# Kernel optimization log

Measured on AMD Instinct MI355X. Metric: run time of the kernel, lower is better.

Reference implementation:

```python
import jax, jax.numpy as jnp
import numpy as np

NUM_HEADS = 16
HEAD_DIM = 64
HIDDEN = NUM_HEADS * HEAD_DIM  # 1024
B, S = 2, 2048
INV_NORM = 1.0 / np.sqrt(HEAD_DIM)


def setup_inputs() -> dict:
    key = jax.random.key(0)
    ks = jax.random.split(key, 8)
    hidden_states = jax.random.normal(ks[0], (1, B, S, HIDDEN), dtype=jnp.float32)
    residual = jax.random.normal(ks[1], (B, S, HIDDEN), dtype=jnp.float32)
    # ALiBi bias per (batch*head) broadcast over query positions: [B*H, 1, S]
    slopes = 2.0 ** (-8.0 * (jnp.arange(1, NUM_HEADS + 1, dtype=jnp.float32) / NUM_HEADS))
    pos = jnp.arange(S, dtype=jnp.float32)
    alibi = (slopes[:, None] * pos[None, :])[None]  # [1, H, S]
    alibi = jnp.broadcast_to(alibi, (B, NUM_HEADS, S)).reshape(B * NUM_HEADS, 1, S)
    # causal mask: True = masked out
    attention_mask = jnp.triu(jnp.ones((S, S), dtype=jnp.bool_), k=1)[None, None]  # [1,1,S,S]
    attention_mask = jnp.broadcast_to(attention_mask, (B, 1, S, S))
    W_qkv = jax.random.normal(ks[2], (3 * HIDDEN, HIDDEN), dtype=jnp.float32) * 0.02
    b_qkv = jax.random.normal(ks[3], (3 * HIDDEN,), dtype=jnp.float32) * 0.02
    W_dense = jax.random.normal(ks[4], (HIDDEN, HIDDEN), dtype=jnp.float32) * 0.02
    b_dense = jax.random.normal(ks[5], (HIDDEN,), dtype=jnp.float32) * 0.02
    return {
        "hidden_states": hidden_states,
        "residual": residual,
        "alibi": alibi,
        "attention_mask": attention_mask,
        "W_qkv": W_qkv,
        "b_qkv": b_qkv,
        "W_dense": W_dense,
        "b_dense": b_dense,
    }


def reference(hidden_states, residual, alibi, attention_mask, W_qkv, b_qkv, W_dense, b_dense):
    x = hidden_states[0]  # [B, S, H]
    b, s, _ = x.shape
    fused = x @ W_qkv.T + b_qkv  # [B, S, 3H]
    # Bloom interleaved split: [B, S, nh, 3, hd]
    qkv = fused.reshape(b, s, NUM_HEADS, 3, HEAD_DIM)
    q = jnp.transpose(qkv[..., 0, :], (0, 2, 1, 3))  # [B, nh, S, hd]
    k = jnp.transpose(qkv[..., 1, :], (0, 2, 1, 3))
    v = jnp.transpose(qkv[..., 2, :], (0, 2, 1, 3))
    # baddbmm: alibi + inv_norm * q @ k^T
    scores = jnp.einsum("bhqd,bhkd->bhqk", q, k) * INV_NORM
    scores = scores + alibi.reshape(b, NUM_HEADS, 1, s)  # [B, nh, S, S]
    neg_min = jnp.finfo(scores.dtype).min
    scores = jnp.where(attention_mask, neg_min, scores)
    probs = jax.nn.softmax(scores.astype(jnp.float32), axis=-1).astype(x.dtype)
    ctx = jnp.einsum("bhqk,bhkd->bhqd", probs, v)  # [B, nh, S, hd]
    ctx = jnp.transpose(ctx, (0, 2, 1, 3)).reshape(b, s, HIDDEN)  # merge_heads
    out = ctx @ W_dense.T + b_dense
    return out + residual  # dropout_add, eval mode
```

## Files before the change

kernel.cpp:

```cpp
#include <hip/hip_runtime.h>
#include <hip/hip_bf16.h>

#define NUM_HEADS 16
#define HEAD_DIM  64
#define HIDDEN    1024
#define BATCH     2
#define SEQ       2048
#define K_DIM     1024
#define INV_NORM  0.125f
#define LOG2E     1.4426950408889634f
#define IN2       (INV_NORM * LOG2E)

typedef __attribute__((ext_vector_type(4)))  float f32x4;
typedef __attribute__((ext_vector_type(16))) float f32x16;
typedef __attribute__((ext_vector_type(8)))  short bf16x8;
typedef __attribute__((ext_vector_type(4)))  unsigned int u32x4;
typedef __attribute__((ext_vector_type(2)))  unsigned int u32x2;
typedef unsigned short u16;

__device__ inline u16 f2bf(float f) {
    __hip_bfloat16 h = __float2bfloat16(f);
    return __builtin_bit_cast(u16, h);
}
__device__ inline float bf2f(u16 u) {
    unsigned int v = ((unsigned int)u) << 16;
    return __builtin_bit_cast(float, v);
}

__device__ inline f32x16 mfma32(bf16x8 a, bf16x8 b, f32x16 c) {
    return __builtin_amdgcn_mfma_f32_32x32x16_bf16(a, b, c, 0, 0, 0);
}

__device__ inline void gl_lds16(const u16* g, u16* s) {
    __builtin_amdgcn_global_load_lds(
        (const __attribute__((address_space(1))) unsigned int*)g,
        (__attribute__((address_space(3))) unsigned int*)s, 16, 0, 0);
}

__device__ inline void pack8(const float* src, u16* dst) {
    const float4 v0 = *reinterpret_cast<const float4*>(src);
    const float4 v1 = *reinterpret_cast<const float4*>(src + 4);
    ushort4 o0, o1;
    o0.x = f2bf(v0.x); o0.y = f2bf(v0.y); o0.z = f2bf(v0.z); o0.w = f2bf(v0.w);
    o1.x = f2bf(v1.x); o1.y = f2bf(v1.y); o1.z = f2bf(v1.z); o1.w = f2bf(v1.w);
    *reinterpret_cast<ushort4*>(dst)     = o0;
    *reinterpret_cast<ushort4*>(dst + 4) = o1;
}
__global__ __launch_bounds__(256) void cvt_all(
        const float* __restrict__ x, const float* __restrict__ wq,
        const float* __restrict__ wd,
        u16* __restrict__ xb, u16* __restrict__ wqb, u16* __restrict__ wdb) {
    int t = blockIdx.x * 256 + threadIdx.x;
    if (t < 524288) {
        int mt = t >> 12, rem = t & 4095;
        int kblk = rem >> 6, hf = (rem >> 5) & 1, ra = rem & 31;
        pack8(x + ((size_t)(mt * 32 + ra)) * K_DIM + kblk * 16 + hf * 8,
              xb + (size_t)t * 8);
    } else if (t < 917504) {
        int t2 = t - 524288;
        int nt = t2 >> 12, rem = t2 & 4095;
        int kblk = rem >> 6, hf = (rem >> 5) & 1, ra = rem & 31;
        pack8(wq + ((size_t)(nt * 32 + ra)) * K_DIM + kblk * 16 + hf * 8,
              wqb + (size_t)t2 * 8);
    } else {
        int i = (t - 917504) * 8;
        pack8(wd + i, wdb + i);
    }
}

#define QLOAD(P, kb) {                                                        \
    P##x0 = *reinterpret_cast<const bf16x8*>(pa0 + (size_t)(kb) * 512);       \
    P##x1 = *reinterpret_cast<const bf16x8*>(pa1 + (size_t)(kb) * 512);       \
    P##y0 = *reinterpret_cast<const bf16x8*>(pb0 + (size_t)(kb) * 512);       \
    P##y1 = *reinterpret_cast<const bf16x8*>(pb1 + (size_t)(kb) * 512);       \
    P##x2 = *reinterpret_cast<const bf16x8*>(pa0 + (size_t)(kb + 1) * 512);   \
    P##x3 = *reinterpret_cast<const bf16x8*>(pa1 + (size_t)(kb + 1) * 512);   \
    P##y2 = *reinterpret_cast<const bf16x8*>(pb0 + (size_t)(kb + 1) * 512);   \
    P##y3 = *reinterpret_cast<const bf16x8*>(pb1 + (size_t)(kb + 1) * 512);   \
}
#define QSTEP(P) {                                                            \
    acc[0][0] = mfma32(P##x0, P##y0, acc[0][0]);                              \
    acc[0][1] = mfma32(P##x0, P##y1, acc[0][1]);                              \
    acc[1][0] = mfma32(P##x1, P##y0, acc[1][0]);                              \
    acc[1][1] = mfma32(P##x1, P##y1, acc[1][1]);                              \
    acc[0][0] = mfma32(P##x2, P##y2, acc[0][0]);                              \
    acc[0][1] = mfma32(P##x2, P##y3, acc[0][1]);                              \
    acc[1][0] = mfma32(P##x3, P##y2, acc[1][0]);                              \
    acc[1][1] = mfma32(P##x3, P##y3, acc[1][1]);                              \
}
__global__ __launch_bounds__(256) void gemm_qkv(
        const u16* __restrict__ Af, const u16* __restrict__ Bf,
        const float* __restrict__ bias,
        u16* __restrict__ qo, u16* __restrict__ ko2, u16* __restrict__ vTo) {
    int lin = blockIdx.x;
    int g = lin & 7, i2 = lin >> 3;
    const int mblk = ((g & 3) * 8 + (i2 & 7)) * 128;
    const int nblk = ((g >> 2) * 12 + (i2 >> 3)) * 128;
    const int tid = threadIdx.x;
    const int w = tid >> 6, lane = tid & 63;
    const int la = lane & 31, hi = lane >> 5;
    const int wr = w >> 1, wc = w & 1;
    const int mt0 = (mblk >> 5) + wr * 2;
    const int nt0 = (nblk >> 5) + wc * 2;
    const u16* pa0 = Af + (size_t)mt0 * 64 * 512 + lane * 8;
    const u16* pa1 = pa0 + 64 * 512;
    const u16* pb0 = Bf + (size_t)nt0 * 64 * 512 + lane * 8;
    const u16* pb1 = pb0 + 64 * 512;
    f32x16 acc[2][2] = {};
    bf16x8 ax0, ax1, ax2, ax3, ay0, ay1, ay2, ay3;
    bf16x8 bx0, bx1, bx2, bx3, by0, by1, by2, by3;
    QLOAD(a, 0)
    #pragma unroll 4
    for (int kb = 0; kb < 64; kb += 4) {
        const int n1 = (kb + 2 < 62) ? kb + 2 : 62;
        QLOAD(b, n1)
        QSTEP(a)
        const int n2 = (kb + 4 < 62) ? kb + 4 : 62;
        QLOAD(a, n2)
        QSTEP(b)
    }
    #pragma unroll
    for (int mi = 0; mi < 2; ++mi)
    #pragma unroll
    for (int ni = 0; ni < 2; ++ni) {
        int c = nblk + wc * 64 + ni * 32 + la;
        int h = c / 192, rem = c - h * 192;
        int which = rem >> 6, d = rem & 63;
        float bv = bias[c];
        #pragma unroll
        for (int r = 0; r < 16; ++r) {
            int m = mblk + wr * 64 + mi * 32 + (r & 3) + 8 * (r >> 2) + 4 * hi;
            int bb = m >> 11, s = m & (SEQ - 1);
            int bh = bb * NUM_HEADS + h;
            int t = s >> 5;
            size_t tb = ((size_t)(bh * 64 + t)) * 2048;
            u16 o = f2bf(acc[mi][ni][r] + bv);
            if (which == 2) {
                int dblk = d >> 5, ra = d & 31;
                int k = s & 31, ks = k >> 4, hf = (k >> 3) & 1, e = k & 7;
                vTo[tb + (dblk * 2 + ks) * 512 + hf * 256 + ra * 8 + e] = o;
            } else {
                int kk = d >> 4, hf = (d >> 3) & 1, e = d & 7, ra = s & 31;
                size_t off = tb + kk * 512 + hf * 256 + ra * 8 + e;
                if (which == 0) qo[off] = o;
                else            ko2[off] = o;
            }
        }
    }
}

__global__ __launch_bounds__(256) void gemm_dense(
        const u16* __restrict__ A, const u16* __restrict__ W,
        const float* __restrict__ bias, const float* __restrict__ residual,
        float* __restrict__ out) {
    __shared__ u16 As[64 * 64];
    __shared__ u16 Bs[128 * 64];
    int lin = blockIdx.x;
    int g = lin & 7, i2 = lin >> 3;
    const int mblk = (g * 8 + (i2 & 7)) * 64;
    const int nblk = (i2 >> 3) * 128;
    const int tid = threadIdx.x;
    const int w = tid >> 6, l = tid & 63;
    const int la = l & 31, hi = l >> 5;
    const int wr = w & 1, wc = w >> 1;
    const int kperm = (((l & 7) ^ (l >> 3)) << 3);
    const u16* gA = A + (size_t)(mblk + w * 16 + (l >> 3)) * K_DIM + kperm;
    const u16* gB = W + (size_t)(nblk + w * 32 + (l >> 3)) * K_DIM + kperm;
    const int sca = (la & 7) << 3;
    f32x16 acc2[2] = {};
    for (int kt = 0; kt < 16; ++kt) {
        const int ko = kt * 64;
        gl_lds16(gA + ko,              &As[(w * 16) * 64]);
        gl_lds16(gA + ko + 8 * K_DIM,  &As[(w * 16 + 8) * 64]);
        #pragma unroll
        for (int i = 0; i < 4; ++i)
            gl_lds16(gB + i * 8 * K_DIM + ko, &Bs[(w * 32 + i * 8) * 64]);
        asm volatile("s_waitcnt vmcnt(0)" ::: "memory");
        __syncthreads();
        const u16* pA = &As[(wr * 32 + la) * 64];
        const u16* pB = &Bs[(wc * 64 + la) * 64];
        #pragma unroll
        for (int kk = 0; kk < 4; ++kk) {
            const int co = (kk * 16 + hi * 8) ^ sca;
            bf16x8 a0 = *reinterpret_cast<const bf16x8*>(pA + co);
            bf16x8 b0 = *reinterpret_cast<const bf16x8*>(pB + co);
            bf16x8 b1 = *reinterpret_cast<const bf16x8*>(pB + 32 * 64 + co);
            acc2[0] = mfma32(a0, b0, acc2[0]);
            acc2[1] = mfma32(a0, b1, acc2[1]);
        }
        __syncthreads();
    }
    #pragma unroll
    for (int ni = 0; ni < 2; ++ni) {
        int c = nblk + wc * 64 + ni * 32 + la;
        float bv = bias[c];
        #pragma unroll
        for (int r = 0; r < 16; ++r) {
            int m = mblk + wr * 32 + (r & 3) + 8 * (r >> 2) + 4 * hi;
            out[(size_t)m * HIDDEN + c] = acc2[ni][r] + bv + residual[(size_t)m * HIDDEN + c];
        }
    }
}

__global__ __launch_bounds__(256) void norms(
        const u16* __restrict__ Kf, const u16* __restrict__ Qf,
        float* __restrict__ knp, float* __restrict__ qn,
        unsigned int* __restrict__ ctr) {
    if (blockIdx.x == 0 && threadIdx.x < 8) ctr[threadIdx.x] = 0;
    __shared__ float red[256];
    const int bh = blockIdx.x >> 3;
    const int s  = (blockIdx.x & 7) * 256 + threadIdx.x;
    const size_t tb = ((size_t)(bh * 64 + (s >> 5))) * 2048 + (s & 31) * 8;
    float ssk = 0.f, ssq = 0.f;
    #pragma unroll
    for (int kk = 0; kk < 4; ++kk)
    #pragma unroll
    for (int hf = 0; hf < 2; ++hf) {
        bf16x8 v = *reinterpret_cast<const bf16x8*>(Kf + tb + kk * 512 + hf * 256);
        bf16x8 u = *reinterpret_cast<const bf16x8*>(Qf + tb + kk * 512 + hf * 256);
        #pragma unroll
        for (int e = 0; e < 8; ++e) {
            float fk = bf2f((u16)v[e]);
            float fq = bf2f((u16)u[e]);
            ssk = fmaf(fk, fk, ssk);
            ssq = fmaf(fq, fq, ssq);
        }
    }
    float mq = ssq;
    #pragma unroll
    for (int off = 1; off <= 16; off <<= 1) mq = fmaxf(mq, __shfl_xor(mq, off));
    if ((threadIdx.x & 31) == 0)
        qn[(size_t)bh * 64 + (s >> 5)] = sqrtf(mq);
    red[threadIdx.x] = ssk;
    __syncthreads();
    for (int off = 128; off; off >>= 1) {
        if (threadIdx.x < (unsigned)off)
            red[threadIdx.x] = fmaxf(red[threadIdx.x], red[threadIdx.x + off]);
        __syncthreads();
    }
    if (threadIdx.x == 0) knp[blockIdx.x] = sqrtf(red[0]);
}

#define LOADT(P, tt) {                                                        \
    const u16* kp_ = kbase + (size_t)(tt) * 2048;                             \
    P##k0 = *reinterpret_cast<const bf16x8*>(kp_);                            \
    P##k1 = *reinterpret_cast<const bf16x8*>(kp_ + 512);                      \
    P##k2 = *reinterpret_cast<const bf16x8*>(kp_ + 1024);                     \
    P##k3 = *reinterpret_cast<const bf16x8*>(kp_ + 1536);                     \
    const u16* vp_ = vbase + (size_t)(tt) * 2048;                             \
    P##v0 = *reinterpret_cast<const bf16x8*>(vp_);                            \
    P##v1 = *reinterpret_cast<const bf16x8*>(vp_ + 512);                      \
    P##v2 = *reinterpret_cast<const bf16x8*>(vp_ + 1024);                     \
    P##v3 = *reinterpret_cast<const bf16x8*>(vp_ + 1536);                     \
}

#define STEP(P, N, tcur, tnxt, DIAG) {                                        \
    f32x16 sca_ = {}, scb_ = {};                                              \
    sca_ = mfma32(P##k0, qf0, sca_);                                          \
    scb_ = mfma32(P##k1, qf1, scb_);                                          \
    sca_ = mfma32(P##k2, qf2, sca_);                                          \
    scb_ = mfma32(P##k3, qf3, scb_);                                          \
    LOADT(N, tnxt)                                                            \
    const float Dt_ = slope2 * (float)((tcur) * 32 - qw);                     \
    float p[16];                                                              \
    _Pragma("unroll")                                                         \
    for (int r = 0; r < 16; ++r)                                              \
        p[r] = __builtin_amdgcn_exp2f(fmaf(sca_[r] + scb_[r], IN2, cl[r] + Dt_)); \
    if (DIAG) {                                                               \
        _Pragma("unroll")                                                     \
        for (int r = 0; r < 16; ++r) {                                        \
            int kr_ = (r & 3) + 8 * (r >> 2) + 4 * hi;                        \
            if (kr_ > la) p[r] = 0.f;                                         \
        }                                                                     \
    }                                                                         \
    l_i += ((p[0] + p[1]) + (p[2] + p[3])) + ((p[4] + p[5]) + (p[6] + p[7]))  \
         + ((p[8] + p[9]) + (p[10] + p[11])) + ((p[12] + p[13]) + (p[14] + p[15])); \
    unsigned pk_[8];                                                          \
    _Pragma("unroll")                                                         \
    for (int m = 0; m < 4; ++m) {                                             \
        unsigned b0_ = __builtin_bit_cast(unsigned, p[4 * m])     + 0x8000u;  \
        unsigned b1_ = __builtin_bit_cast(unsigned, p[4 * m + 1]) + 0x8000u;  \
        unsigned b2_ = __builtin_bit_cast(unsigned, p[4 * m + 2]) + 0x8000u;  \
        unsigned b3_ = __builtin_bit_cast(unsigned, p[4 * m + 3]) + 0x8000u;  \
        pk_[2 * m]     = __builtin_amdgcn_perm(b1_, b0_, 0x07060302u);        \
        pk_[2 * m + 1] = __builtin_amdgcn_perm(b3_, b2_, 0x07060302u);        \
    }                                                                         \
    u32x2 r0_ = __builtin_amdgcn_permlane32_swap(pk_[0], pk_[2], false, false); \
    u32x2 r1_ = __builtin_amdgcn_permlane32_swap(pk_[1], pk_[3], false, false); \
    u32x2 r2_ = __builtin_amdgcn_permlane32_swap(pk_[4], pk_[6], false, false); \
    u32x2 r3_ = __builtin_amdgcn_permlane32_swap(pk_[5], pk_[7], false, false); \
    u32x4 pb0_, pb1_;                                                         \
    pb0_[0] = r0_[0]; pb0_[1] = r1_[0]; pb0_[2] = r0_[1]; pb0_[3] = r1_[1];   \
    pb1_[0] = r2_[0]; pb1_[1] = r3_[0]; pb1_[2] = r2_[1]; pb1_[3] = r3_[1];   \
    bf16x8 pf0_ = __builtin_bit_cast(bf16x8, pb0_);                           \
    bf16x8 pf1_ = __builtin_bit_cast(bf16x8, pb1_);                           \
    o0 = mfma32(P##v0, pf0_, o0);                                             \
    o0 = mfma32(P##v1, pf1_, o0);                                             \
    o1 = mfma32(P##v2, pf0_, o1);                                             \
    o1 = mfma32(P##v3, pf1_, o1);                                             \
}

__global__ __launch_bounds__(256) void attn(
        const u16* __restrict__ Qf, const u16* __restrict__ Kf,
        const u16* __restrict__ Vf, const float* __restrict__ alibi,
        const float* __restrict__ knp, const float* __restrict__ qn,
        u16* __restrict__ ctx, unsigned int* __restrict__ ctr) {
    __shared__ float o_l[4][64][33];
    __shared__ float ml[4][32];
    __shared__ unsigned int s_idx;
    const int grp  = blockIdx.x & 7;
    const int lst  = grp >> 1;
    const int bat  = grp & 1;
    const unsigned long long LH = (lst == 0) ? 0x0000000007080Full
                               : (lst == 1) ? 0x000000000006090Eull
                               : (lst == 2) ? 0x0000000003050A0Dull
                                            : 0x00000102040B0Cull;
    const unsigned nit = (lst == 0) ? 192u : (lst == 3) ? 320u : 256u;
    const int wave = __builtin_amdgcn_readfirstlane(threadIdx.x >> 6);
    const int lane = threadIdx.x & 63;
    const int la = lane & 31, hi = lane >> 5;

    for (;;) {
        if (threadIdx.x == 0) s_idx = atomicAdd(ctr + grp, 1u);
        __syncthreads();
        const unsigned int idx = s_idx;
        if (idx >= nit) return;
        const int h  = (int)((LH >> (8 * (idx >> 6))) & 0xFF);
        const int qt = 63 - (int)(idx & 63);
        const int bh = bat * 16 + h;
        const int qw = qt * 32;
        const size_t tbh = (size_t)bh * 64;
        const float slope2 = alibi[(size_t)bh * SEQ + 1] * LOG2E;

        const u16* qp = Qf + (tbh + qt) * 2048 + lane * 8;
        bf16x8 qf0 = *reinterpret_cast<const bf16x8*>(qp);
        bf16x8 qf1 = *reinterpret_cast<const bf16x8*>(qp + 512);
        bf16x8 qf2 = *reinterpret_cast<const bf16x8*>(qp + 1024);
        bf16x8 qf3 = *reinterpret_cast<const bf16x8*>(qp + 1536);

        const u16* kbase = Kf + tbh * 2048 + lane * 8;
        const u16* vbase = Vf + tbh * 2048 + lane * 8;
        const int t0 = qt - wave;
        const int ta = (t0 >= 0) ? t0 : 0;
        bf16x8 ak0, ak1, ak2, ak3, av0, av1, av2, av3;
        bf16x8 bk0, bk1, bk2, bk3, bv0, bv1, bv2, bv3;
        bf16x8 ck0, ck1, ck2, ck3, cv0, cv1, cv2, cv3;
        LOADT(a, ta)

        const float* kp8 = knp + bh * 8;
        const float knv = fmaxf(fmaxf(fmaxf(kp8[0], kp8[1]), fmaxf(kp8[2], kp8[3])),
                                fmaxf(fmaxf(kp8[4], kp8[5]), fmaxf(kp8[6], kp8[7])));
        const float kb = qn[tbh + qt] * knv * IN2;

        const float Wf = (47.f + 2.f * kb) / slope2;
        const int lo_k = qw - 31 - (int)Wf;
        const int t_lo = lo_k <= 0 ? 0 : ((lo_k + 31) >> 5);

        float cl[16];
        #pragma unroll
        for (int r = 0; r < 16; ++r)
            cl[r] = slope2 * (float)((r & 3) + 8 * (r >> 2) + 4 * hi - la) - kb;

        f32x16 o0 = {}, o1 = {};
        float l_i = 0.f;

        if (t0 >= t_lo) {
            const int nit2 = ((t0 - t_lo) >> 2) + 1;
            const int tlast = t0 - 4 * (nit2 - 1);
            const int t1 = (nit2 > 1) ? t0 - 4 : t0;
            LOADT(b, t1)
            {
                const int t2c = (nit2 > 2) ? t0 - 8 : tlast;
                if (wave == 0) { STEP(a, c, t0, t2c, 1) }
                else           { STEP(a, c, t0, t2c, 0) }
            }
            int i = 1;
            while (i < nit2) {
                {
                    const int tc = t0 - 4 * i;
                    const int tn = (i + 2 < nit2) ? tc - 8 : tlast;
                    STEP(b, a, tc, tn, 0)
                }
                ++i;
                if (i >= nit2) break;
                {
                    const int tc = t0 - 4 * i;
                    const int tn = (i + 2 < nit2) ? tc - 8 : tlast;
                    STEP(c, b, tc, tn, 0)
                }
                ++i;
                if (i >= nit2) break;
                {
                    const int tc = t0 - 4 * i;
                    const int tn = (i + 2 < nit2) ? tc - 8 : tlast;
                    STEP(a, c, tc, tn, 0)
                }
                ++i;
            }
        }

        l_i += __shfl_xor(l_i, 32);
        if (hi == 0) ml[wave][la] = l_i;
        #pragma unroll
        for (int r = 0; r < 16; ++r) {
            int d = (r & 3) + 8 * (r >> 2) + 4 * hi;
            o_l[wave][d][la]      = o0[r];
            o_l[wave][d + 32][la] = o1[r];
        }
        __syncthreads();

        const int qq = threadIdx.x >> 3;
        const int d0 = (threadIdx.x & 7) * 8;
        float L = ml[0][qq] + ml[1][qq] + ml[2][qq] + ml[3][qq];
        float inv = 1.0f / L;
        unsigned int packed[4];
        #pragma unroll
        for (int e2 = 0; e2 < 4; ++e2) {
            float Oa = o_l[0][d0 + 2 * e2][qq] + o_l[1][d0 + 2 * e2][qq]
                     + o_l[2][d0 + 2 * e2][qq] + o_l[3][d0 + 2 * e2][qq];
            float Ob = o_l[0][d0 + 2 * e2 + 1][qq] + o_l[1][d0 + 2 * e2 + 1][qq]
                     + o_l[2][d0 + 2 * e2 + 1][qq] + o_l[3][d0 + 2 * e2 + 1][qq];
            packed[e2] = (unsigned)f2bf(Oa * inv) | ((unsigned)f2bf(Ob * inv) << 16);
        }
        const int bb = bh >> 4, hh = bh & 15;
        u32x4 pv; pv[0] = packed[0]; pv[1] = packed[1]; pv[2] = packed[2]; pv[3] = packed[3];
        *reinterpret_cast<u32x4*>(
            &ctx[((size_t)(bb * SEQ + qw + qq)) * HIDDEN + hh * HEAD_DIM + d0]) = pv;
    }
}

extern "C" void kernel_launch(void* const* d_in, const int* in_sizes, int n_in,
                              void* d_out, int out_size, void* d_ws, size_t ws_size,
                              hipStream_t stream) {
    const float* x        = (const float*)d_in[0];
    const float* residual = (const float*)d_in[1];
    const float* alibi    = (const float*)d_in[2];
    const float* W_qkv    = (const float*)d_in[4];
    const float* b_qkv    = (const float*)d_in[5];
    const float* W_dense  = (const float*)d_in[6];
    const float* b_dense  = (const float*)d_in[7];
    float* out = (float*)d_out;

    char* ws = (char*)d_ws;
    u16* xb  = (u16*)(ws);
    u16* wqb = (u16*)(ws + 8388608);
    u16* wdb = (u16*)(ws + 14680064);
    u16* q   = (u16*)(ws + 16777216);
    u16* k   = (u16*)(ws + 25165824);
    u16* vT  = (u16*)(ws + 33554432);
    u16* ctx = (u16*)(ws + 41943040);
    float* knp = (float*)(ws + 50331648);
    float* qn  = (float*)(ws + 50331648 + 1024);
    unsigned int* ctr = (unsigned int*)(ws + 50331648 + 16384);

    cvt_all<<<4096, 256, 0, stream>>>(x, W_qkv, W_dense, xb, wqb, wdb);
    gemm_qkv<<<768, 256, 0, stream>>>(xb, wqb, b_qkv, q, k, vT);
    norms<<<256, 256, 0, stream>>>(k, q, knp, qn, ctr);
    attn<<<1024, 256, 0, stream>>>(q, k, vT, alibi, knp, qn, ctx, ctr);
    gemm_dense<<<512, 256, 0, stream>>>(ctx, wdb, b_dense, residual, out);
}
```

Baseline: 121.8 us.

## Cut attention register and LDS pressure to raise occupancy, launch more blocks

The attention kernel goes from triple-buffered to double-buffered K/V register prefetch and drops the per-row cl[16] array by computing the ALiBi offset inline from a constant plus a scalar. It derives the V pointer from the K pointer through a fixed workspace offset. It halves the LDS reduction buffer by reducing the two output halves in two passes with an extra barrier. The grid grows from 1024 to 1280 persistent blocks, aiming to fit more resident waves per CU. The trade-offs are a shorter prefetch distance, which can expose load latency, and extra synchronisation in the epilogue.

```diff
diff --git a/kernel.cpp b/kernel.cpp
--- a/kernel.cpp
+++ b/kernel.cpp
@@ -247,7 +247,7 @@
     P##k1 = *reinterpret_cast<const bf16x8*>(kp_ + 512);                      \
     P##k2 = *reinterpret_cast<const bf16x8*>(kp_ + 1024);                     \
     P##k3 = *reinterpret_cast<const bf16x8*>(kp_ + 1536);                     \
-    const u16* vp_ = vbase + (size_t)(tt) * 2048;                             \
+    const u16* vp_ = kp_ + 4194304;                                           \
     P##v0 = *reinterpret_cast<const bf16x8*>(vp_);                            \
     P##v1 = *reinterpret_cast<const bf16x8*>(vp_ + 512);                      \
     P##v2 = *reinterpret_cast<const bf16x8*>(vp_ + 1024);                     \
@@ -261,11 +261,14 @@
     sca_ = mfma32(P##k2, qf2, sca_);                                          \
     scb_ = mfma32(P##k3, qf3, scb_);                                          \
     LOADT(N, tnxt)                                                            \
-    const float Dt_ = slope2 * (float)((tcur) * 32 - qw);                     \
+    const float base_ = fmaf(slope2, (float)((tcur) * 32 - qw), C0);          \
     float p[16];                                                              \
     _Pragma("unroll")                                                         \
-    for (int r = 0; r < 16; ++r)                                              \
-        p[r] = __builtin_amdgcn_exp2f(fmaf(sca_[r] + scb_[r], IN2, cl[r] + Dt_)); \
+    for (int r = 0; r < 16; ++r) {                                            \
+        const float cst_ = (float)((r & 3) + 8 * (r >> 2));                   \
+        p[r] = __builtin_amdgcn_exp2f(                                        \
+            fmaf(sca_[r] + scb_[r], IN2, fmaf(cst_, slope2, base_)));         \
+    }                                                                         \
     if (DIAG) {                                                               \
         _Pragma("unroll")                                                     \
         for (int r = 0; r < 16; ++r) {                                        \
@@ -305,7 +308,7 @@
         const u16* __restrict__ Vf, const float* __restrict__ alibi,
         const float* __restrict__ knp, const float* __restrict__ qn,
         u16* __restrict__ ctx, unsigned int* __restrict__ ctr) {
-    __shared__ float o_l[4][64][33];
+    __shared__ float o_l[4][32][33];
     __shared__ float ml[4][32];
     __shared__ unsigned int s_idx;
     const int grp  = blockIdx.x & 7;
@@ -339,61 +342,45 @@
         bf16x8 qf3 = *reinterpret_cast<const bf16x8*>(qp + 1536);
 
         const u16* kbase = Kf + tbh * 2048 + lane * 8;
-        const u16* vbase = Vf + tbh * 2048 + lane * 8;
         const int t0 = qt - wave;
         const int ta = (t0 >= 0) ? t0 : 0;
         bf16x8 ak0, ak1, ak2, ak3, av0, av1, av2, av3;
         bf16x8 bk0, bk1, bk2, bk3, bv0, bv1, bv2, bv3;
-        bf16x8 ck0, ck1, ck2, ck3, cv0, cv1, cv2, cv3;
         LOADT(a, ta)
 
         const float* kp8 = knp + bh * 8;
         const float knv = fmaxf(fmaxf(fmaxf(kp8[0], kp8[1]), fmaxf(kp8[2], kp8[3])),
                                 fmaxf(fmaxf(kp8[4], kp8[5]), fmaxf(kp8[6], kp8[7])));
         const float kb = qn[tbh + qt] * knv * IN2;
+        const float C0 = fmaf(slope2, (float)(4 * hi - la), -kb);
 
         const float Wf = (47.f + 2.f * kb) / slope2;
         const int lo_k = qw - 31 - (int)Wf;
         const int t_lo = lo_k <= 0 ? 0 : ((lo_k + 31) >> 5);
 
-        float cl[16];
-        #pragma unroll
-        for (int r = 0; r < 16; ++r)
-            cl[r] = slope2 * (float)((r & 3) + 8 * (r >> 2) + 4 * hi - la) - kb;
-
         f32x16 o0 = {}, o1 = {};
         float l_i = 0.f;
 
         if (t0 >= t_lo) {
             const int nit2 = ((t0 - t_lo) >> 2) + 1;
-            const int tlast = t0 - 4 * (nit2 - 1);
-            const int t1 = (nit2 > 1) ? t0 - 4 : t0;
-            LOADT(b, t1)
             {
-                const int t2c = (nit2 > 2) ? t0 - 8 : tlast;
-                if (wave == 0) { STEP(a, c, t0, t2c, 1) }
-                else           { STEP(a, c, t0, t2c, 0) }
+                const int tn1 = (nit2 > 1) ? t0 - 4 : t0;
+                if (wave == 0) { STEP(a, b, t0, tn1, 1) }
+                else           { STEP(a, b, t0, tn1, 0) }
             }
             int i = 1;
             while (i < nit2) {
                 {
                     const int tc = t0 - 4 * i;
-                    const int tn = (i + 2 < nit2) ? tc - 8 : tlast;
+                    const int tn = (i + 1 < nit2) ? tc - 4 : tc;
                     STEP(b, a, tc, tn, 0)
                 }
                 ++i;
                 if (i >= nit2) break;
                 {
                     const int tc = t0 - 4 * i;
-                    const int tn = (i + 2 < nit2) ? tc - 8 : tlast;
-                    STEP(c, b, tc, tn, 0)
-                }
-                ++i;
-                if (i >= nit2) break;
-                {
-                    const int tc = t0 - 4 * i;
-                    const int tn = (i + 2 < nit2) ? tc - 8 : tlast;
-                    STEP(a, c, tc, tn, 0)
+                    const int tn = (i + 1 < nit2) ? tc - 4 : tc;
+                    STEP(a, b, tc, tn, 0)
                 }
                 ++i;
             }
@@ -402,30 +389,44 @@
         l_i += __shfl_xor(l_i, 32);
         if (hi == 0) ml[wave][la] = l_i;
         #pragma unroll
-        for (int r = 0; r < 16; ++r) {
-            int d = (r & 3) + 8 * (r >> 2) + 4 * hi;
-            o_l[wave][d][la]      = o0[r];
-            o_l[wave][d + 32][la] = o1[r];
-        }
-        __syncthreads();
-
+        for (int r = 0; r < 16; ++r)
+            o_l[wave][(r & 3) + 8 * (r >> 2) + 4 * hi][la] = o0[r];
+        __syncthreads();
         const int qq = threadIdx.x >> 3;
-        const int d0 = (threadIdx.x & 7) * 8;
-        float L = ml[0][qq] + ml[1][qq] + ml[2][qq] + ml[3][qq];
-        float inv = 1.0f / L;
-        unsigned int packed[4];
-        #pragma unroll
-        for (int e2 = 0; e2 < 4; ++e2) {
-            float Oa = o_l[0][d0 + 2 * e2][qq] + o_l[1][d0 + 2 * e2][qq]
-                     + o_l[2][d0 + 2 * e2][qq] + o_l[3][d0 + 2 * e2][qq];
-            float Ob = o_l[0][d0 + 2 * e2 + 1][qq] + o_l[1][d0 + 2 * e2 + 1][qq]
-                     + o_l[2][d0 + 2 * e2 + 1][qq] + o_l[3][d0 + 2 * e2 + 1][qq];
-            packed[e2] = (unsigned)f2bf(Oa * inv) | ((unsigned)f2bf(Ob * inv) << 16);
-        }
+        const int ds = (threadIdx.x & 7) * 4;
+        const float L = ml[0][qq] + ml[1][qq] + ml[2][qq] + ml[3][qq];
+        const float inv = 1.0f / L;
         const int bb = bh >> 4, hh = bh & 15;
-        u32x4 pv; pv[0] = packed[0]; pv[1] = packed[1]; pv[2] = packed[2]; pv[3] = packed[3];
-        *reinterpret_cast<u32x4*>(
-            &ctx[((size_t)(bb * SEQ + qw + qq)) * HIDDEN + hh * HEAD_DIM + d0]) = pv;
+        u16* crow = &ctx[((size_t)(bb * SEQ + qw + qq)) * HIDDEN + hh * HEAD_DIM];
+        {
+            u32x2 pv;
+            #pragma unroll
+            for (int e2 = 0; e2 < 2; ++e2) {
+                float Oa = o_l[0][ds + 2 * e2][qq] + o_l[1][ds + 2 * e2][qq]
+                         + o_l[2][ds + 2 * e2][qq] + o_l[3][ds + 2 * e2][qq];
+                float Ob = o_l[0][ds + 2 * e2 + 1][qq] + o_l[1][ds + 2 * e2 + 1][qq]
+                         + o_l[2][ds + 2 * e2 + 1][qq] + o_l[3][ds + 2 * e2 + 1][qq];
+                pv[e2] = (unsigned)f2bf(Oa * inv) | ((unsigned)f2bf(Ob * inv) << 16);
+            }
+            *reinterpret_cast<u32x2*>(crow + ds) = pv;
+        }
+        __syncthreads();
+        #pragma unroll
+        for (int r = 0; r < 16; ++r)
+            o_l[wave][(r & 3) + 8 * (r >> 2) + 4 * hi][la] = o1[r];
+        __syncthreads();
+        {
+            u32x2 pv;
+            #pragma unroll
+            for (int e2 = 0; e2 < 2; ++e2) {
+                float Oa = o_l[0][ds + 2 * e2][qq] + o_l[1][ds + 2 * e2][qq]
+                         + o_l[2][ds + 2 * e2][qq] + o_l[3][ds + 2 * e2][qq];
+                float Ob = o_l[0][ds + 2 * e2 + 1][qq] + o_l[1][ds + 2 * e2 + 1][qq]
+                         + o_l[2][ds + 2 * e2 + 1][qq] + o_l[3][ds + 2 * e2 + 1][qq];
+                pv[e2] = (unsigned)f2bf(Oa * inv) | ((unsigned)f2bf(Ob * inv) << 16);
+            }
+            *reinterpret_cast<u32x2*>(crow + 32 + ds) = pv;
+        }
     }
 }
 
@@ -456,6 +457,6 @@
     cvt_all<<<4096, 256, 0, stream>>>(x, W_qkv, W_dense, xb, wqb, wdb);
     gemm_qkv<<<768, 256, 0, stream>>>(xb, wqb, b_qkv, q, k, vT);
     norms<<<256, 256, 0, stream>>>(k, q, knp, qn, ctr);
-    attn<<<1024, 256, 0, stream>>>(q, k, vT, alibi, knp, qn, ctx, ctr);
+    attn<<<1280, 256, 0, stream>>>(q, k, vT, alibi, knp, qn, ctx, ctr);
     gemm_dense<<<512, 256, 0, stream>>>(ctx, wdb, b_dense, residual, out);
 }
```

Measured after the change: 127.2 us. +4.4%, slower.

## Process two adjacent query tiles per work item to reuse K/V loads

Applied to the files above, without the earlier changes.

Each work item in the attention kernel now handles a pair of adjacent 32-row query tiles instead of one. Every K/V tile loaded from memory feeds both query tiles' score MFMAs and softmax/PV steps, which halves K/V global traffic per query and halves the number of work items and atomic fetches. The prefetch pipeline drops from triple to double buffering to offset the extra registers used by the second set of Q fragments and accumulators. This raises register pressure and may lower occupancy, and the epilogue now runs twice with additional barriers.

```diff
diff --git a/kernel.cpp b/kernel.cpp
--- a/kernel.cpp
+++ b/kernel.cpp
@@ -254,34 +254,30 @@
     P##v3 = *reinterpret_cast<const bf16x8*>(vp_ + 1536);                     \
 }
 
-#define STEP(P, N, tcur, tnxt, DIAG) {                                        \
-    f32x16 sca_ = {}, scb_ = {};                                              \
-    sca_ = mfma32(P##k0, qf0, sca_);                                          \
-    scb_ = mfma32(P##k1, qf1, scb_);                                          \
-    sca_ = mfma32(P##k2, qf2, sca_);                                          \
-    scb_ = mfma32(P##k3, qf3, scb_);                                          \
-    LOADT(N, tnxt)                                                            \
-    const float Dt_ = slope2 * (float)((tcur) * 32 - qw);                     \
-    float p[16];                                                              \
+#define SMPV(SA, SB, BASEX, DIAGX, LI, OA, OB, P) {                           \
+    float p_[16];                                                             \
     _Pragma("unroll")                                                         \
-    for (int r = 0; r < 16; ++r)                                              \
-        p[r] = __builtin_amdgcn_exp2f(fmaf(sca_[r] + scb_[r], IN2, cl[r] + Dt_)); \
-    if (DIAG) {                                                               \
+    for (int r = 0; r < 16; ++r) {                                            \
+        const float cst_ = (float)((r & 3) + 8 * (r >> 2));                   \
+        p_[r] = __builtin_amdgcn_exp2f(                                       \
+            fmaf(SA[r] + SB[r], IN2, fmaf(cst_, slope2, BASEX)));             \
+    }                                                                         \
+    if (DIAGX) {                                                              \
         _Pragma("unroll")                                                     \
         for (int r = 0; r < 16; ++r) {                                        \
             int kr_ = (r & 3) + 8 * (r >> 2) + 4 * hi;                        \
-            if (kr_ > la) p[r] = 0.f;                                         \
+            if (kr_ > la) p_[r] = 0.f;                                        \
         }                                                                     \
     }                                                                         \
-    l_i += ((p[0] + p[1]) + (p[2] + p[3])) + ((p[4] + p[5]) + (p[6] + p[7]))  \
-         + ((p[8] + p[9]) + (p[10] + p[11])) + ((p[12] + p[13]) + (p[14] + p[15])); \
+    LI += ((p_[0] + p_[1]) + (p_[2] + p_[3])) + ((p_[4] + p_[5]) + (p_[6] + p_[7]))   \
+        + ((p_[8] + p_[9]) + (p_[10] + p_[11])) + ((p_[12] + p_[13]) + (p_[14] + p_[15])); \
     unsigned pk_[8];                                                          \
     _Pragma("unroll")                                                         \
     for (int m = 0; m < 4; ++m) {                                             \
-        unsigned b0_ = __builtin_bit_cast(unsigned, p[4 * m])     + 0x8000u;  \
-        unsigned b1_ = __builtin_bit_cast(unsigned, p[4 * m + 1]) + 0x8000u;  \
-        unsigned b2_ = __builtin_bit_cast(unsigned, p[4 * m + 2]) + 0x8000u;  \
-        unsigned b3_ = __builtin_bit_cast(unsigned, p[4 * m + 3]) + 0x8000u;  \
+        unsigned b0_ = __builtin_bit_cast(unsigned, p_[4 * m])     + 0x8000u; \
+        unsigned b1_ = __builtin_bit_cast(unsigned, p_[4 * m + 1]) + 0x8000u; \
+        unsigned b2_ = __builtin_bit_cast(unsigned, p_[4 * m + 2]) + 0x8000u; \
+        unsigned b3_ = __builtin_bit_cast(unsigned, p_[4 * m + 3]) + 0x8000u; \
         pk_[2 * m]     = __builtin_amdgcn_perm(b1_, b0_, 0x07060302u);        \
         pk_[2 * m + 1] = __builtin_amdgcn_perm(b3_, b2_, 0x07060302u);        \
     }                                                                         \
@@ -294,10 +290,35 @@
     pb1_[0] = r2_[0]; pb1_[1] = r3_[0]; pb1_[2] = r2_[1]; pb1_[3] = r3_[1];   \
     bf16x8 pf0_ = __builtin_bit_cast(bf16x8, pb0_);                           \
     bf16x8 pf1_ = __builtin_bit_cast(bf16x8, pb1_);                           \
-    o0 = mfma32(P##v0, pf0_, o0);                                             \
-    o0 = mfma32(P##v1, pf1_, o0);                                             \
-    o1 = mfma32(P##v2, pf0_, o1);                                             \
-    o1 = mfma32(P##v3, pf1_, o1);                                             \
+    OA = mfma32(P##v0, pf0_, OA);                                             \
+    OA = mfma32(P##v1, pf1_, OA);                                             \
+    OB = mfma32(P##v2, pf0_, OB);                                             \
+    OB = mfma32(P##v3, pf1_, OB);                                             \
+}
+
+#define STEP2(P, N, tcur, tnxt, DIAGH, DOLO, DIAGL) {                         \
+    const int k0_ = (tcur) * 32;                                              \
+    f32x16 sha_ = {}, shb_ = {};                                              \
+    sha_ = mfma32(P##k0, qfh0, sha_);                                         \
+    shb_ = mfma32(P##k1, qfh1, shb_);                                         \
+    sha_ = mfma32(P##k2, qfh2, sha_);                                         \
+    shb_ = mfma32(P##k3, qfh3, shb_);                                         \
+    f32x16 sla_ = {}, slb_ = {};                                              \
+    if (DOLO) {                                                               \
+        sla_ = mfma32(P##k0, qfl0, sla_);                                     \
+        slb_ = mfma32(P##k1, qfl1, slb_);                                     \
+        sla_ = mfma32(P##k2, qfl2, sla_);                                     \
+        slb_ = mfma32(P##k3, qfl3, slb_);                                     \
+    }                                                                         \
+    LOADT(N, tnxt)                                                            \
+    {                                                                         \
+        const float baseh_ = fmaf(slope2, (float)(k0_ - qw_hi), C0 - kb_h);   \
+        SMPV(sha_, shb_, baseh_, DIAGH, l_h, o0h, o1h, P)                     \
+    }                                                                         \
+    if (DOLO) {                                                               \
+        const float basel_ = fmaf(slope2, (float)(k0_ - qw_lo), C0 - kb_l);   \
+        SMPV(sla_, slb_, basel_, DIAGL, l_l, o0l, o1l, P)                     \
+    }                                                                         \
 }
 
 __global__ __launch_bounds__(256) void attn(
@@ -315,7 +336,7 @@
                                : (lst == 1) ? 0x000000000006090Eull
                                : (lst == 2) ? 0x0000000003050A0Dull
                                             : 0x00000102040B0Cull;
-    const unsigned nit = (lst == 0) ? 192u : (lst == 3) ? 320u : 256u;
+    const unsigned nit = (lst == 0) ? 96u : (lst == 3) ? 160u : 128u;
     const int wave = __builtin_amdgcn_readfirstlane(threadIdx.x >> 6);
     const int lane = threadIdx.x & 63;
     const int la = lane & 31, hi = lane >> 5;
@@ -325,107 +346,133 @@
         __syncthreads();
         const unsigned int idx = s_idx;
         if (idx >= nit) return;
-        const int h  = (int)((LH >> (8 * (idx >> 6))) & 0xFF);
-        const int qt = 63 - (int)(idx & 63);
+        const int h  = (int)((LH >> (8 * (idx >> 5))) & 0xFF);
+        const int pr = (int)(idx & 31u);
+        const int qt_hi = 63 - 2 * pr;
+        const int qt_lo = qt_hi - 1;
         const int bh = bat * 16 + h;
-        const int qw = qt * 32;
+        const int qw_hi = qt_hi * 32;
+        const int qw_lo = qw_hi - 32;
         const size_t tbh = (size_t)bh * 64;
         const float slope2 = alibi[(size_t)bh * SEQ + 1] * LOG2E;
 
-        const u16* qp = Qf + (tbh + qt) * 2048 + lane * 8;
-        bf16x8 qf0 = *reinterpret_cast<const bf16x8*>(qp);
-        bf16x8 qf1 = *reinterpret_cast<const bf16x8*>(qp + 512);
-        bf16x8 qf2 = *reinterpret_cast<const bf16x8*>(qp + 1024);
-        bf16x8 qf3 = *reinterpret_cast<const bf16x8*>(qp + 1536);
+        const u16* qph = Qf + (tbh + qt_hi) * 2048 + lane * 8;
+        bf16x8 qfh0 = *reinterpret_cast<const bf16x8*>(qph);
+        bf16x8 qfh1 = *reinterpret_cast<const bf16x8*>(qph + 512);
+        bf16x8 qfh2 = *reinterpret_cast<const bf16x8*>(qph + 1024);
+        bf16x8 qfh3 = *reinterpret_cast<const bf16x8*>(qph + 1536);
+        const u16* qpl = qph - 2048;
+        bf16x8 qfl0 = *reinterpret_cast<const bf16x8*>(qpl);
+        bf16x8 qfl1 = *reinterpret_cast<const bf16x8*>(qpl + 512);
+        bf16x8 qfl2 = *reinterpret_cast<const bf16x8*>(qpl + 1024);
+        bf16x8 qfl3 = *reinterpret_cast<const bf16x8*>(qpl + 1536);
 
         const u16* kbase = Kf + tbh * 2048 + lane * 8;
         const u16* vbase = Vf + tbh * 2048 + lane * 8;
-        const int t0 = qt - wave;
+        const int t0 = qt_hi - wave;
         const int ta = (t0 >= 0) ? t0 : 0;
         bf16x8 ak0, ak1, ak2, ak3, av0, av1, av2, av3;
         bf16x8 bk0, bk1, bk2, bk3, bv0, bv1, bv2, bv3;
-        bf16x8 ck0, ck1, ck2, ck3, cv0, cv1, cv2, cv3;
         LOADT(a, ta)
 
         const float* kp8 = knp + bh * 8;
         const float knv = fmaxf(fmaxf(fmaxf(kp8[0], kp8[1]), fmaxf(kp8[2], kp8[3])),
                                 fmaxf(fmaxf(kp8[4], kp8[5]), fmaxf(kp8[6], kp8[7])));
-        const float kb = qn[tbh + qt] * knv * IN2;
-
-        const float Wf = (47.f + 2.f * kb) / slope2;
-        const int lo_k = qw - 31 - (int)Wf;
-        const int t_lo = lo_k <= 0 ? 0 : ((lo_k + 31) >> 5);
-
-        float cl[16];
-        #pragma unroll
-        for (int r = 0; r < 16; ++r)
-            cl[r] = slope2 * (float)((r & 3) + 8 * (r >> 2) + 4 * hi - la) - kb;
-
-        f32x16 o0 = {}, o1 = {};
-        float l_i = 0.f;
-
-        if (t0 >= t_lo) {
-            const int nit2 = ((t0 - t_lo) >> 2) + 1;
-            const int tlast = t0 - 4 * (nit2 - 1);
+        const float kb_h = qn[tbh + qt_hi] * knv * IN2;
+        const float kb_l = qn[tbh + qt_lo] * knv * IN2;
+        const float C0 = slope2 * (float)(4 * hi - la);
+
+        const float Wh = (47.f + 2.f * kb_h) / slope2;
+        const float Wl = (47.f + 2.f * kb_l) / slope2;
+        const int lo_kh = qw_hi - 31 - (int)Wh;
+        const int lo_kl = qw_lo - 31 - (int)Wl;
+        const int t_lh = lo_kh <= 0 ? 0 : ((lo_kh + 31) >> 5);
+        const int t_ll = lo_kl <= 0 ? 0 : ((lo_kl + 31) >> 5);
+        const int t_min = (t_lh < t_ll) ? t_lh : t_ll;
+
+        f32x16 o0h = {}, o1h = {}, o0l = {}, o1l = {};
+        float l_h = 0.f, l_l = 0.f;
+
+        if (t0 >= t_min) {
+            const int nit2 = ((t0 - t_min) >> 2) + 1;
             const int t1 = (nit2 > 1) ? t0 - 4 : t0;
-            LOADT(b, t1)
-            {
-                const int t2c = (nit2 > 2) ? t0 - 8 : tlast;
-                if (wave == 0) { STEP(a, c, t0, t2c, 1) }
-                else           { STEP(a, c, t0, t2c, 0) }
-            }
+            if (wave == 0)      { STEP2(a, b, t0, t1, 1, 0, 0) }
+            else if (wave == 1) { STEP2(a, b, t0, t1, 0, 1, 1) }
+            else                { STEP2(a, b, t0, t1, 0, 1, 0) }
             int i = 1;
             while (i < nit2) {
                 {
                     const int tc = t0 - 4 * i;
-                    const int tn = (i + 2 < nit2) ? tc - 8 : tlast;
-                    STEP(b, a, tc, tn, 0)
+                    const int tn = (i + 1 < nit2) ? tc - 4 : tc;
+                    STEP2(b, a, tc, tn, 0, 1, 0)
                 }
                 ++i;
                 if (i >= nit2) break;
                 {
                     const int tc = t0 - 4 * i;
-                    const int tn = (i + 2 < nit2) ? tc - 8 : tlast;
-                    STEP(c, b, tc, tn, 0)
-                }
-                ++i;
-                if (i >= nit2) break;
-                {
-                    const int tc = t0 - 4 * i;
-                    const int tn = (i + 2 < nit2) ? tc - 8 : tlast;
-                    STEP(a, c, tc, tn, 0)
+                    const int tn = (i + 1 < nit2) ? tc - 4 : tc;
+                    STEP2(a, b, tc, tn, 0, 1, 0)
                 }
                 ++i;
             }
         }
 
-        l_i += __shfl_xor(l_i, 32);
-        if (hi == 0) ml[wave][la] = l_i;
+        const int qq = threadIdx.x >> 3;
+        const int d0 = (threadIdx.x & 7) * 8;
+        const int bb = bh >> 4, hh = bh & 15;
+
+        l_h += __shfl_xor(l_h, 32);
+        if (hi == 0) ml[wave][la] = l_h;
         #pragma unroll
         for (int r = 0; r < 16; ++r) {
             int d = (r & 3) + 8 * (r >> 2) + 4 * hi;
-            o_l[wave][d][la]      = o0[r];
-            o_l[wave][d + 32][la] = o1[r];
-        }
-        __syncthreads();
-
-        const int qq = threadIdx.x >> 3;
-        const int d0 = (threadIdx.x & 7) * 8;
-        float L = ml[0][qq] + ml[1][qq] + ml[2][qq] + ml[3][qq];
-        float inv = 1.0f / L;
-        unsigned int packed[4];
-        #pragma unroll
-        for (int e2 = 0; e2 < 4; ++e2) {
-            float Oa = o_l[0][d0 + 2 * e2][qq] + o_l[1][d0 + 2 * e2][qq]
-                     + o_l[2][d0 + 2 * e2][qq] + o_l[3][d0 + 2 * e2][qq];
-            float Ob = o_l[0][d0 + 2 * e2 + 1][qq] + o_l[1][d0 + 2 * e2 + 1][qq]
-                     + o_l[2][d0 + 2 * e2 + 1][qq] + o_l[3][d0 + 2 * e2 + 1][qq];
-            packed[e2] = (unsigned)f2bf(Oa * inv) | ((unsigned)f2bf(Ob * inv) << 16);
-        }
-        const int bb = bh >> 4, hh = bh & 15;
-        u32x4 pv; pv[0] = packed[0]; pv[1] = packed[1]; pv[2] = packed[2]; pv[3] = packed[3];
-        *reinterpret_cast<u32x4*>(
-            &ctx[((size_t)(bb * SEQ + qw + qq)) * HIDDEN + hh * HEAD_DIM + d0]) = pv;
+            o_l[wave][d][la]      = o0h[r];
+            o_l[wave][d + 32][la] = o1h[r];
+        }
+        __syncthreads();
+        {
+            float L = ml[0][qq] + ml[1][qq] + ml[2][qq] + ml[3][qq];
+            float inv = 1.0f / L;
+            unsigned int packed[4];
+            #pragma unroll
+            for (int e2 = 0; e2 < 4; ++e2) {
+                float Oa = o_l[0][d0 + 2 * e2][qq] + o_l[1][d0 + 2 * e2][qq]
+                         + o_l[2][d0 + 2 * e2][qq] + o_l[3][d0 + 2 * e2][qq];
+                float Ob = o_l[0][d0 + 2 * e2 + 1][qq] + o_l[1][d0 + 2 * e2 + 1][qq]
+                         + o_l[2][d0 + 2 * e2 + 1][qq] + o_l[3][d0 + 2 * e2 + 1][qq];
+                packed[e2] = (unsigned)f2bf(Oa * inv) | ((unsigned)f2bf(Ob * inv) << 16);
+            }
+            u32x4 pv; pv[0] = packed[0]; pv[1] = packed[1]; pv[2] = packed[2]; pv[3] = packed[3];
+            *reinterpret_cast<u32x4*>(
+                &ctx[((size_t)(bb * SEQ + qw_hi + qq)) * HIDDEN + hh * HEAD_DIM + d0]) = pv;
+        }
+        __syncthreads();
+
+        l_l += __shfl_xor(l_l, 32);
+        if (hi == 0) ml[wave][la] = l_l;
+        #pragma unroll
+        for (int r = 0; r < 16; ++r) {
+            int d = (r & 3) + 8 * (r >> 2) + 4 * hi;
+            o_l[wave][d][la]      = o0l[r];
+            o_l[wave][d + 32][la] = o1l[r];
+        }
+        __syncthreads();
+        {
+            float L = ml[0][qq] + ml[1][qq] + ml[2][qq] + ml[3][qq];
+            float inv = 1.0f / L;
+            unsigned int packed[4];
+            #pragma unroll
+            for (int e2 = 0; e2 < 4; ++e2) {
+                float Oa = o_l[0][d0 + 2 * e2][qq] + o_l[1][d0 + 2 * e2][qq]
+                         + o_l[2][d0 + 2 * e2][qq] + o_l[3][d0 + 2 * e2][qq];
+                float Ob = o_l[0][d0 + 2 * e2 + 1][qq] + o_l[1][d0 + 2 * e2 + 1][qq]
+                         + o_l[2][d0 + 2 * e2 + 1][qq] + o_l[3][d0 + 2 * e2 + 1][qq];
+                packed[e2] = (unsigned)f2bf(Oa * inv) | ((unsigned)f2bf(Ob * inv) << 16);
+            }
+            u32x4 pv; pv[0] = packed[0]; pv[1] = packed[1]; pv[2] = packed[2]; pv[3] = packed[3];
+            *reinterpret_cast<u32x4*>(
+                &ctx[((size_t)(bb * SEQ + qw_lo + qq)) * HIDDEN + hh * HEAD_DIM + d0]) = pv;
+        }
     }
 }
 
```

Measured after the change: 120.7 us. No clear change (-0.9%).
